# Performance work log

Hardware: AMD Instinct MI355X
Metric: run time of the kernel (lower is better)

## Reference

```python
import jax, jax.numpy as jnp
import numpy as np

B, S, T = 32, 64, 64          # batch, src_len, tgt_len
E = 1024                      # embedding_dim
H = 512                       # encoder hidden per direction
H2 = 2 * H                    # decoder hidden = enc_output_dim = 1024
VS, VT = 32000, 32000         # src / tgt vocab
L_ENC, L_DEC = 2, 2


def setup_inputs() -> dict:
    key = jax.random.key(0)
    ks = jax.random.split(key, 16)
    s = 0.05
    return {
        # tokens in [1, V) -> no pad tokens, all src_lens == S
        "x": jax.random.randint(ks[0], (B, S), 1, VS),
        "y": jax.random.randint(ks[1], (B, T), 1, VT),
        "src_emb": jax.random.normal(ks[2], (VS, E), jnp.float32) * s,
        "tgt_emb": jax.random.normal(ks[3], (VT, E), jnp.float32) * s,
        # encoder weights: [layer, dir(0=fwd,1=bwd), 4H, in] with in = E = 2H
        "enc_W_ih": jax.random.normal(ks[4], (L_ENC, 2, 4 * H, E), jnp.float32) * s,
        "enc_W_hh": jax.random.normal(ks[5], (L_ENC, 2, 4 * H, H), jnp.float32) * s,
        "enc_b_ih": jax.random.normal(ks[6], (L_ENC, 2, 4 * H), jnp.float32) * s,
        "enc_b_hh": jax.random.normal(ks[7], (L_ENC, 2, 4 * H), jnp.float32) * s,
        # decoder LSTMCells: cell0 input = E + H2 = 2048, cell1 input = H2
        "dec_W_ih0": jax.random.normal(ks[8], (4 * H2, E + H2), jnp.float32) * s,
        "dec_W_ih1": jax.random.normal(ks[9], (4 * H2, H2), jnp.float32) * s,
        "dec_W_hh": jax.random.normal(ks[10], (L_DEC, 4 * H2, H2), jnp.float32) * s,
        "dec_b_ih": jax.random.normal(ks[11], (L_DEC, 4 * H2), jnp.float32) * s,
        "dec_b_hh": jax.random.normal(ks[12], (L_DEC, 4 * H2), jnp.float32) * s,
        "W_out": jax.random.normal(ks[13], (VT, H2), jnp.float32) * s,
        "b_out": jax.random.normal(ks[14], (VT,), jnp.float32) * s,
    }


def _lstm_cell(x, h, c, W_ih, W_hh, b):
    # PyTorch gate order: i, f, g, o
    gates = x @ W_ih.T + h @ W_hh.T + b
    i, f, g, o = jnp.split(gates, 4, axis=-1)
    c2 = jax.nn.sigmoid(f) * c + jax.nn.sigmoid(i) * jnp.tanh(g)
    h2 = jax.nn.sigmoid(o) * jnp.tanh(c2)
    return h2, c2


def _run_dir(xseq, W_ih, W_hh, b):
    # xseq: [T, B, D] -> outputs [T, B, H], final (h, c)
    Bn, Hn = xseq.shape[1], W_hh.shape[1]
    init = (jnp.zeros((Bn, Hn), xseq.dtype), jnp.zeros((Bn, Hn), xseq.dtype))
    def step(carry, xt):
        h, c = carry
        h2, c2 = _lstm_cell(xt, h, c, W_ih, W_hh, b)
        return (h2, c2), h2
    (hT, cT), ys = jax.lax.scan(step, init, xseq)
    return ys, hT, cT


def _forward(x, y, src_emb, tgt_emb, enc_W_ih, enc_W_hh, enc_b_ih, enc_b_hh,
             dec_W_ih0, dec_W_ih1, dec_W_hh, dec_b_ih, dec_b_hh, W_out, b_out):
    # All src lengths are full -> per-row flip == full flip (pack is a no-op).
    x_rev = jnp.flip(x, axis=1)
    seq = src_emb[x_rev].transpose(1, 0, 2)  # [S, B, E]; dropout=0 (eval)

    h_fin, c_fin = [], []
    for l in range(L_ENC):
        b_f = enc_b_ih[l, 0] + enc_b_hh[l, 0]
        b_b = enc_b_ih[l, 1] + enc_b_hh[l, 1]
        ys_f, hT_f, cT_f = _run_dir(seq, enc_W_ih[l, 0], enc_W_hh[l, 0], b_f)
        ys_b, hT_b, cT_b = _run_dir(seq[::-1], enc_W_ih[l, 1], enc_W_hh[l, 1], b_b)
        seq = jnp.concatenate([ys_f, ys_b[::-1]], axis=-1)  # [S, B, 2H]
        h_fin.append(jnp.concatenate([hT_f, hT_b], axis=-1))  # [B, 2H]
        c_fin.append(jnp.concatenate([cT_f, cT_b], axis=-1))

    context = h_fin[-1]  # cat(hidden[-2], hidden[-1]) = last-layer fwd||bwd

    db0 = dec_b_ih[0] + dec_b_hh[0]
    db1 = dec_b_ih[1] + dec_b_hh[1]
    emb_seq = tgt_emb[y[:, :-1]].transpose(1, 0, 2)  # [T-1, B, E] teacher forcing

    def dec_step(carry, emb_t):
        h0, c0, h1, c1 = carry
        inp0 = jnp.concatenate([emb_t, context], axis=-1)
        h0, c0 = _lstm_cell(inp0, h0, c0, dec_W_ih0, dec_W_hh[0], db0)
        h1, c1 = _lstm_cell(h0, h1, c1, dec_W_ih1, dec_W_hh[1], db1)
        logit = h1 @ W_out.T + b_out
        return (h0, c0, h1, c1), logit

    init = (h_fin[0], c_fin[0], h_fin[1], c_fin[1])
    _, logits = jax.lax.scan(dec_step, init, emb_seq)  # [T-1, B, VT]
    return logits.transpose(1, 0, 2)  # [B, T-1, VT]


def reference(x, y, src_emb, tgt_emb, enc_W_ih, enc_W_hh, enc_b_ih, enc_b_hh,
              dec_W_ih0, dec_W_ih1, dec_W_hh, dec_b_ih, dec_b_hh, W_out, b_out):
    return _forward(x, y, src_emb, tgt_emb, enc_W_ih, enc_W_hh, enc_b_ih, enc_b_hh,
                    dec_W_ih0, dec_W_ih1, dec_W_hh, dec_b_ih, dec_b_hh, W_out, b_out)
```

## Files before the change

### kernel.cpp

```cpp
#include <hip/hip_runtime.h>

typedef __attribute__((ext_vector_type(8))) short short8;
typedef __attribute__((ext_vector_type(4))) float f32x4;

#define DEVINL __device__ __forceinline__

DEVINL unsigned short f2bf(float f) {
  unsigned int u = __builtin_bit_cast(unsigned int, f);
  unsigned int r = u + 0x7FFFu + ((u >> 16) & 1u);
  return (unsigned short)(r >> 16);
}
DEVINL float bf2f(unsigned short u) {
  unsigned int x = ((unsigned int)u) << 16;
  return __builtin_bit_cast(float, x);
}
DEVINL float sig_(float x) { return 1.f / (1.f + __expf(-x)); }
DEVINL float tanh_(float x) { return 2.f / (1.f + __expf(-2.f * x)) - 1.f; }

DEVINL void gld16(void* lds, const void* g) {
  __builtin_amdgcn_global_load_lds(
      (const __attribute__((address_space(1))) unsigned int*)g,
      (__attribute__((address_space(3))) unsigned int*)lds, 16, 0, 0);
}

DEVINL void coh_st(unsigned long long* p, unsigned long long v) {
  __hip_atomic_store(p, v, __ATOMIC_RELAXED, __HIP_MEMORY_SCOPE_AGENT);
}

DEVINL unsigned long long pack4w(unsigned int u, int lane, int s0, int s1) {
  unsigned int p1 = (unsigned int)__shfl_xor((int)u, s0);
  unsigned int lo2 = (lane & s0) ? ((p1 & 0xFFFFu) | (u << 16))
                                 : ((u & 0xFFFFu) | (p1 << 16));
  unsigned int p2 = (unsigned int)__shfl_xor((int)lo2, s1);
  unsigned int lo = (lane & s1) ? p2 : lo2;
  unsigned int hi = (lane & s1) ? lo2 : p2;
  return ((unsigned long long)hi << 32) | lo;
}

DEVINL void bar_arrive(int* arr, int idx, int gen) {
  if (threadIdx.x == 0)
    __hip_atomic_store(arr + idx, gen, __ATOMIC_RELAXED, __HIP_MEMORY_SCOPE_AGENT);
}
DEVINL void bar_wait(const int* arr, int nb, int gen) {
  if (threadIdx.x < 64) {
    for (;;) {
      int ok = 1;
      for (int i = (int)threadIdx.x; i < nb; i += 64)
        ok &= (__hip_atomic_load(arr + i, __ATOMIC_RELAXED, __HIP_MEMORY_SCOPE_AGENT) >= gen)
                  ? 1
                  : 0;
      if (__all(ok)) break;
      __builtin_amdgcn_s_sleep(2);
    }
  }
  __builtin_amdgcn_sched_barrier(0);
  asm volatile("" ::: "memory");
  __syncthreads();
}

__global__ __launch_bounds__(256) void gemm_bf16(
    const unsigned short* __restrict__ A, const unsigned short* __restrict__ Bt,
    void* __restrict__ C, const float* __restrict__ bias,
    int K, int N, int Mvalid, int mode) {
  __shared__ unsigned short lA[1024 * 8];
  __shared__ unsigned short lB[1024 * 8];
  const int tid = threadIdx.x;
  const int lane = tid & 63, wid = tid >> 6;
  const int wm = wid >> 1, wn = wid & 1;
  const int bm = blockIdx.x, bn = blockIdx.y;
  const size_t K_ = (size_t)K;

  const unsigned short* gAc[4];
  const unsigned short* gBc[4];
  unsigned short* lAc[4];
  unsigned short* lBc[4];
#pragma unroll
  for (int c = 0; c < 4; c++) {
    const int s = c * 256 + tid;
    const int r = s & 127, kb = s >> 7;
    gAc[c] = A + (size_t)(bm * 128 + r) * K_ + kb * 8;
    gBc[c] = Bt + (size_t)(bn * 128 + r) * K_ + kb * 8;
    lAc[c] = lA + (size_t)(c * 256 + wid * 64) * 8;
    lBc[c] = lB + (size_t)(c * 256 + wid * 64) * 8;
  }

  f32x4 acc[4][4] = {};
  const int kg = lane >> 4, lr = lane & 15;

  for (int kt = 0; kt < K; kt += 64) {
#pragma unroll
    for (int c = 0; c < 4; c++) {
      gld16(lAc[c], gAc[c] + kt);
      gld16(lBc[c], gBc[c] + kt);
    }
    __syncthreads();
#pragma unroll
    for (int ks = 0; ks < 2; ks++) {
      const int kgi = ks * 4 + kg;
      short8 af[4], bfr[4];
#pragma unroll
      for (int fm = 0; fm < 4; fm++)
        af[fm] = *(const short8*)&lA[(size_t)(kgi * 128 + wm * 64 + fm * 16 + lr) * 8];
#pragma unroll
      for (int fn = 0; fn < 4; fn++)
        bfr[fn] = *(const short8*)&lB[(size_t)(kgi * 128 + wn * 64 + fn * 16 + lr) * 8];
#pragma unroll
      for (int fm = 0; fm < 4; fm++)
#pragma unroll
        for (int fn = 0; fn < 4; fn++)
          acc[fm][fn] =
              __builtin_amdgcn_mfma_f32_16x16x32_bf16(af[fm], bfr[fn], acc[fm][fn], 0, 0, 0);
    }
    __syncthreads();
  }

#pragma unroll
  for (int fn = 0; fn < 4; fn++) {
    const int col = bn * 128 + wn * 64 + fn * 16 + lr;
    const float bv = bias ? bias[col] : 0.f;
#pragma unroll
    for (int fm = 0; fm < 4; fm++) {
      const int row0 = bm * 128 + wm * 64 + fm * 16 + kg * 4;
#pragma unroll
      for (int r = 0; r < 4; r++) {
        const int m = row0 + r;
        if (m < Mvalid) {
          const float v = acc[fm][fn][r] + bv;
          if (mode == 0) {
            ((float*)C)[(size_t)m * N + col] = v;
          } else if (mode == 1) {
            const int b = m & 31, t = m >> 5;
            ((float*)C)[(size_t)b * 2016000 + (size_t)t * 32000 + col] = v;
          } else {
            ((unsigned short*)C)[(size_t)m * N + col] = f2bf(v);
          }
        }
      }
    }
  }
}

__global__ __launch_bounds__(128, 1) void enc_chain(
    const unsigned short* __restrict__ Whh, const unsigned short* __restrict__ G,
    unsigned short* __restrict__ Henc, unsigned short* __restrict__ seq_out,
    float* __restrict__ c_out, int* bar) {
  extern __shared__ unsigned short lw[];
  const int tid = threadIdx.x, lane = tid & 63, w = tid >> 6;
  const int lr = lane & 15, kg = lane >> 4;
  const int dir = (int)blockIdx.x >> 4, j0 = ((int)blockIdx.x & 15) * 32;
  int* arr = bar + dir * 64;
  const int aidx = (int)blockIdx.x & 15;
  const unsigned short* Wd = Whh + (size_t)dir * 2048 * 512;
  for (int it = 0; it < 64; it++) {
    const int idx = (it * 128 + tid) * 16;
    const int r = idx >> 10, o = idx & 1023;
    const unsigned short* src = Wd + (size_t)((r >> 5) * 512 + j0 + (r & 31)) * 512 + (o >> 1);
    *(short8*)((char*)lw + r * 1024 + (o ^ ((r & 7) << 4))) = *(const short8*)src;
  }
  float cc[2][4] = {};
  float gpre[4][2][4];
  auto fetch_g = [&](int t) {
    const int s_idx = dir ? (63 - t) : t;
#pragma unroll
    for (int r = 0; r < 4; r++) {
      const unsigned short* Gr =
          G + (size_t)(s_idx * 32 + (w * 16 + kg * 4 + r)) * 4096 + dir * 2048;
#pragma unroll
      for (int jh = 0; jh < 2; jh++) {
        const int jj = j0 + jh * 16 + lr;
        gpre[r][jh][0] = bf2f(Gr[jj]);
        gpre[r][jh][1] = bf2f(Gr[512 + jj]);
        gpre[r][jh][2] = bf2f(Gr[1024 + jj]);
        gpre[r][jh][3] = bf2f(Gr[1536 + jj]);
      }
    }
  };
  fetch_g(0);
  __syncthreads();
  for (int t = 0; t < 64; t++) {
    const unsigned short* hA =
        Henc + ((size_t)(t * 2 + dir) * 32 + w * 16 + lr) * 512 + kg * 8;
    short8 areg[16];
#pragma unroll
    for (int kc = 0; kc < 16; kc++) areg[kc] = *(const short8*)(hA + kc * 32);
    f32x4 acc[8] = {};
#pragma unroll
    for (int kc = 0; kc < 16; kc++)
#pragma unroll
      for (int nt = 0; nt < 8; nt++) {
        const int rr = nt * 16 + lr;
        short8 bf = *(const short8*)((const char*)lw + rr * 1024 +
                                     ((kc * 64 + kg * 16) ^ ((rr & 7) << 4)));
        acc[nt] = __builtin_amdgcn_mfma_f32_16x16x32_bf16(areg[kc], bf, acc[nt], 0, 0, 0);
      }
    const int s_idx = dir ? (63 - t) : t;
    unsigned long long* HWU =
        (unsigned long long*)Henc + ((size_t)((t + 1) * 2 + dir) * 32) * 128;
#pragma unroll
    for (int r = 0; r < 4; r++) {
      const int b = w * 16 + kg * 4 + r;
#pragma unroll
      for (int jh = 0; jh < 2; jh++) {
        const float gi = gpre[r][jh][0] + acc[jh + 0][r];
        const float gf = gpre[r][jh][1] + acc[jh + 2][r];
        const float gg = gpre[r][jh][2] + acc[jh + 4][r];
        const float go = gpre[r][jh][3] + acc[jh + 6][r];
        const float cn = sig_(gf) * cc[jh][r] + sig_(gi) * tanh_(gg);
        const float hn = sig_(go) * tanh_(cn);
        cc[jh][r] = cn;
        unsigned long long pk = pack4w((unsigned int)f2bf(hn), lane, 1, 2);
        if ((lane & 3) == 0) {
          const int jjb = j0 + jh * 16 + lr;
          coh_st(HWU + b * 128 + (jjb >> 2), pk);
          if (seq_out)
            *(unsigned long long*)&seq_out[(size_t)(s_idx * 32 + b) * 1024 + dir * 512 +
                                           jjb] = pk;
        }
      }
    }
    if (t < 63) {
      __syncthreads();
      bar_arrive(arr, aidx, t + 1);
      fetch_g(t + 1);
      bar_wait(arr, 16, t + 1);
    }
  }
#pragma unroll
  for (int r = 0; r < 4; r++)
#pragma unroll
    for (int jh = 0; jh < 2; jh++)
      c_out[(dir * 32 + (w * 16 + kg * 4 + r)) * 512 + j0 + jh * 16 + lr] = cc[jh][r];
}

__global__ __launch_bounds__(128, 1) void dec_pipe(
    const unsigned short* __restrict__ Whh0, const unsigned short* __restrict__ Wc1,
    const unsigned short* __restrict__ G, const float* __restrict__ db1,
    const float* __restrict__ c0init, const float* __restrict__ c1init,
    unsigned short* __restrict__ H0ext, unsigned short* __restrict__ H1ext,
    int* bar) {
  extern __shared__ unsigned short lw[];
  const int tid = threadIdx.x, lane = tid & 63, w = tid >> 6;
  const int lr = lane & 15, kg = lane >> 4;
  const int bid = (int)blockIdx.x;

  if (bid < 64) {
    const int j0 = bid * 16, j = j0 + lr;
    for (int it = 0; it < 64; it++) {
      const int idx = (it * 128 + tid) * 16;
      const int r = idx >> 11, o = idx & 2047;
      const unsigned short* src =
          Whh0 + (size_t)((r >> 4) * 1024 + j0 + (r & 15)) * 1024 + (o >> 1);
      *(short8*)((char*)lw + r * 2048 + (o ^ ((r & 7) << 4))) = *(const short8*)src;
    }
    float cc[4];
#pragma unroll
    for (int r = 0; r < 4; r++) cc[r] = c0init[(w * 16 + kg * 4 + r) * 1024 + j];
    float gpre[4][4];
    auto fetch_g = [&](int k) {
#pragma unroll
      for (int r = 0; r < 4; r++) {
        const unsigned short* Gr = G + (size_t)(k * 32 + (w * 16 + kg * 4 + r)) * 4096 + j;
        gpre[r][0] = bf2f(Gr[0]);
        gpre[r][1] = bf2f(Gr[1024]);
        gpre[r][2] = bf2f(Gr[2048]);
        gpre[r][3] = bf2f(Gr[3072]);
      }
    };
    fetch_g(0);
    __syncthreads();
    for (int k = 0; k < 64; k++) {
      if (k < 63) {
        const unsigned short* hA = H0ext + ((size_t)k * 32 + w * 16 + lr) * 1024 + kg * 8;
        short8 areg[32];
#pragma unroll
        for (int kc = 0; kc < 32; kc++) areg[kc] = *(const short8*)(hA + kc * 32);
        f32x4 acc[4] = {};
#pragma unroll
        for (int kc = 0; kc < 32; kc++)
#pragma unroll
          for (int g = 0; g < 4; g++) {
            const int rr = g * 16 + lr;
            short8 bf = *(const short8*)((const char*)lw + rr * 2048 +
                                         ((kc * 64 + kg * 16) ^ ((rr & 7) << 4)));
            acc[g] = __builtin_amdgcn_mfma_f32_16x16x32_bf16(areg[kc], bf, acc[g], 0, 0, 0);
          }
        unsigned long long* HWU = (unsigned long long*)H0ext + ((size_t)(k + 1) * 32) * 256;
#pragma unroll
        for (int r = 0; r < 4; r++) {
          const int b = w * 16 + kg * 4 + r;
          const float gi = gpre[r][0] + acc[0][r];
          const float gf = gpre[r][1] + acc[1][r];
          const float gg = gpre[r][2] + acc[2][r];
          const float go = gpre[r][3] + acc[3][r];
          const float cn = sig_(gf) * cc[r] + sig_(gi) * tanh_(gg);
          const float hn = sig_(go) * tanh_(cn);
          cc[r] = cn;
          unsigned long long pk = pack4w((unsigned int)f2bf(hn), lane, 1, 2);
          if ((lane & 3) == 0)
            coh_st(HWU + b * 256 + ((j0 + lr) >> 2), pk);
        }
      }
      if (k < 63) {
        __syncthreads();
        bar_arrive(bar, bid, k + 1);
        if (k < 62) fetch_g(k + 1);
        bar_wait(bar, 192, k + 1);
      }
    }
  } else {
    const int j0 = (bid - 64) * 8;
    for (int it = 0; it < 64; it++) {
      const int idx = (it * 128 + tid) * 16;
      const int r = idx >> 12, o = idx & 4095;
      const unsigned short* src =
          Wc1 + (size_t)((r & 3) * 1024 + j0 + (r >> 2)) * 2048 + (o >> 1);
      *(short8*)((char*)lw + r * 4096 + (o ^ ((r & 7) << 4))) = *(const short8*)src;
    }
    float cc[2][4];
    float bb1[2][4];
#pragma unroll
    for (int n = 0; n < 2; n++) {
      const int j = j0 + n * 4 + (lr >> 2);
#pragma unroll
      for (int g = 0; g < 4; g++) bb1[n][g] = db1[g * 1024 + j];
#pragma unroll
      for (int r = 0; r < 4; r++)
        cc[n][r] = c1init[(w * 16 + kg * 4 + r) * 1024 + j];
    }
    __syncthreads();
    for (int k = 0; k < 64; k++) {
      if (k >= 1) {
        f32x4 acc[2] = {};
        {
          const unsigned short* hA = H0ext + ((size_t)k * 32 + w * 16 + lr) * 1024 + kg * 8;
          short8 areg[32];
#pragma unroll
          for (int kc = 0; kc < 32; kc++) areg[kc] = *(const short8*)(hA + kc * 32);
#pragma unroll
          for (int kc = 0; kc < 32; kc++)
#pragma unroll
            for (int n = 0; n < 2; n++) {
              const int rr = n * 16 + lr;
              short8 bf = *(const short8*)((const char*)lw + rr * 4096 +
                                           ((kc * 64 + kg * 16) ^ ((rr & 7) << 4)));
              acc[n] = __builtin_amdgcn_mfma_f32_16x16x32_bf16(areg[kc], bf, acc[n], 0, 0, 0);
            }
        }
        {
          const unsigned short* hA =
              H1ext + ((size_t)(k - 1) * 32 + w * 16 + lr) * 1024 + kg * 8;
          short8 areg[32];
#pragma unroll
          for (int kc = 0; kc < 32; kc++) areg[kc] = *(const short8*)(hA + kc * 32);
#pragma unroll
          for (int kc = 32; kc < 64; kc++)
#pragma unroll
            for (int n = 0; n < 2; n++) {
              const int rr = n * 16 + lr;
              short8 bf = *(const short8*)((const char*)lw + rr * 4096 +
                                           ((kc * 64 + kg * 16) ^ ((rr & 7) << 4)));
              acc[n] = __builtin_amdgcn_mfma_f32_16x16x32_bf16(areg[kc - 32], bf, acc[n],
                                                               0, 0, 0);
            }
        }
        unsigned long long* HWU = (unsigned long long*)H1ext + ((size_t)k * 32) * 256;
#pragma unroll
        for (int n = 0; n < 2; n++) {
#pragma unroll
          for (int r = 0; r < 4; r++) {
            const int b = w * 16 + kg * 4 + r;
            const float v = acc[n][r];
            const float e1a = __shfl_xor(v, 1);
            const float e0 = (lane & 1) ? e1a : v;
            const float e1 = (lane & 1) ? v : e1a;
            const float f0 = __shfl_xor(e0, 2), f1 = __shfl_xor(e1, 2);
            const float gi = ((lane & 2) ? f0 : e0) + bb1[n][0];
            const float gf = ((lane & 2) ? f1 : e1) + bb1[n][1];
            const float gg = ((lane & 2) ? e0 : f0) + bb1[n][2];
            const float go = ((lane & 2) ? e1 : f1) + bb1[n][3];
            const float cn = sig_(gf) * cc[n][r] + sig_(gi) * tanh_(gg);
            const float hn = sig_(go) * tanh_(cn);
            cc[n][r] = cn;
            unsigned long long pk = pack4w((unsigned int)f2bf(hn), lane, 4, 8);
            if ((lane & 15) == 0)
              coh_st(HWU + b * 256 + ((j0 + n * 4) >> 2), pk);
          }
        }
      }
      if (k < 63) {
        __syncthreads();
        bar_arrive(bar, bid, k + 1);
        bar_wait(bar, 192, k + 1);
      }
    }
  }
}

__global__ void cvt_bf16(const float* __restrict__ in, unsigned short* __restrict__ out,
                         long n4) {
  long i = (long)blockIdx.x * blockDim.x + threadIdx.x;
  const long stride = (long)gridDim.x * blockDim.x;
  for (; i < n4; i += stride) {
    f32x4 v = *(const f32x4*)&in[i * 4];
    ushort4 o = {f2bf(v.x), f2bf(v.y), f2bf(v.z), f2bf(v.w)};
    *(ushort4*)&out[i * 4] = o;
  }
}

__global__ void pack_wc1(const float* __restrict__ Wih1, const float* __restrict__ Whh1,
                         unsigned short* __restrict__ Wc) {
  const int n = blockIdx.x;
  const int c = threadIdx.x * 8;
  const float* src = (c < 1024) ? (Wih1 + (size_t)n * 1024 + c)
                                : (Whh1 + (size_t)n * 1024 + (c - 1024));
  f32x4 v0 = *(const f32x4*)src;
  f32x4 v1 = *(const f32x4*)(src + 4);
  ushort4 o0 = {f2bf(v0.x), f2bf(v0.y), f2bf(v0.z), f2bf(v0.w)};
  ushort4 o1 = {f2bf(v1.x), f2bf(v1.y), f2bf(v1.z), f2bf(v1.w)};
  *(ushort4*)&Wc[(size_t)n * 2048 + c] = o0;
  *(ushort4*)&Wc[(size_t)n * 2048 + c + 4] = o1;
}

__global__ void bias_comb(const float* __restrict__ a, const float* __restrict__ b,
                          float* __restrict__ out, int n) {
  int i = blockIdx.x * blockDim.x + threadIdx.x;
  if (i < n) out[i] = a[i] + b[i];
}

__global__ void embed_src(const int* __restrict__ x, const float* __restrict__ emb,
                          unsigned short* __restrict__ A0) {
  const int row = blockIdx.x;
  const int s = row >> 5, b = row & 31;
  const int tok = x[b * 64 + (63 - s)];
  const int col = threadIdx.x * 4;
  f32x4 v = *(const f32x4*)(emb + (size_t)tok * 1024 + col);
  ushort4 o = {f2bf(v.x), f2bf(v.y), f2bf(v.z), f2bf(v.w)};
  *(ushort4*)&A0[(size_t)row * 1024 + col] = o;
}

__global__ void embed_tgt(const int* __restrict__ y, const float* __restrict__ emb,
                          unsigned short* __restrict__ inp0) {
  const int row = blockIdx.x;
  const int col = threadIdx.x * 4;
  ushort4 o = {0, 0, 0, 0};
  if (row < 2016) {
    const int t = row >> 5, b = row & 31;
    const int tok = y[b * 64 + t];
    f32x4 v = *(const f32x4*)(emb + (size_t)tok * 1024 + col);
    o = ushort4{f2bf(v.x), f2bf(v.y), f2bf(v.z), f2bf(v.w)};
  } else {
    *(ushort4*)&inp0[(size_t)row * 2048 + 1024 + col] = o;
  }
  *(ushort4*)&inp0[(size_t)row * 2048 + col] = o;
}

__global__ void fill_ctx2(const unsigned short* __restrict__ Hl1,
                          unsigned short* __restrict__ inp0) {
  const int row = blockIdx.x;
  const int b = row & 31;
  const int col = threadIdx.x * 4;
  const int dir = col >> 9, jj = col & 511;
  ushort4 v = *(const ushort4*)(Hl1 + ((size_t)dir * 32 + b) * 512 + jj);
  *(ushort4*)&inp0[(size_t)row * 2048 + 1024 + col] = v;
}

__global__ void dec_init2(const unsigned short* __restrict__ Hl0,
                          const unsigned short* __restrict__ Hl1,
                          const float* __restrict__ Cl0, const float* __restrict__ Cl1,
                          unsigned short* __restrict__ H0e, unsigned short* __restrict__ H1e,
                          float* __restrict__ c0, float* __restrict__ c1) {
  const int i = blockIdx.x * 256 + threadIdx.x;
  const int b = i >> 10, col = i & 1023;
  const int dir = col >> 9, jj = col & 511;
  const int se = (dir * 32 + b) * 512 + jj;
  const int de = b * 1024 + col;
  H0e[de] = Hl0[se];
  H1e[de] = Hl1[se];
  c0[de] = Cl0[se];
  c1[de] = Cl1[se];
}

extern "C" void kernel_launch(void* const* d_in, const int* in_sizes, int n_in,
                              void* d_out, int out_size, void* d_ws, size_t ws_size,
                              hipStream_t stream) {
  const int* x = (const int*)d_in[0];
  const int* y = (const int*)d_in[1];
  const float* src_emb = (const float*)d_in[2];
  const float* tgt_emb = (const float*)d_in[3];
  const float* enc_W_ih = (const float*)d_in[4];
  const float* enc_W_hh = (const float*)d_in[5];
  const float* enc_b_ih = (const float*)d_in[6];
  const float* enc_b_hh = (const float*)d_in[7];
  const float* dec_W_ih0 = (const float*)d_in[8];
  const float* dec_W_ih1 = (const float*)d_in[9];
  const float* dec_W_hh = (const float*)d_in[10];
  const float* dec_b_ih = (const float*)d_in[11];
  const float* dec_b_hh = (const float*)d_in[12];
  const float* W_out = (const float*)d_in[13];
  const float* b_out = (const float*)d_in[14];
  float* out = (float*)d_out;

  char* ws = (char*)d_ws;
  size_t off = 0;
  auto alloc = [&](size_t bytes) -> void* {
    void* p = ws + off;
    off += (bytes + 255) & ~(size_t)255;
    return p;
  };
  unsigned short* A0 = (unsigned short*)alloc(2048ull * 1024 * 2);
  unsigned short* seq1 = (unsigned short*)alloc(2048ull * 1024 * 2);
  unsigned short* Wih_bf = (unsigned short*)alloc(2ull * 4096 * 1024 * 2);
  unsigned short* Wih0_bf = (unsigned short*)alloc(4096ull * 2048 * 2);
  unsigned short* Wout_bf = (unsigned short*)alloc(32000ull * 1024 * 2);
  unsigned short* G = (unsigned short*)alloc(2048ull * 4096 * 2);
  unsigned short* inp0 = (unsigned short*)alloc(2048ull * 2048 * 2);
  unsigned short* Whh_enc_bf = (unsigned short*)alloc(2ull * 2 * 2048 * 512 * 2);
  unsigned short* Whh0_bf = (unsigned short*)alloc(4096ull * 1024 * 2);
  unsigned short* Wc1_bf = (unsigned short*)alloc(4096ull * 2048 * 2);
  unsigned short* H0ext = (unsigned short*)alloc(2080ull * 1024 * 2);
  unsigned short* H1ext = (unsigned short*)alloc(2080ull * 1024 * 2);
  unsigned short* Henc0 = (unsigned short*)alloc(65ull * 2 * 32 * 512 * 2);
  unsigned short* Henc1 = (unsigned short*)alloc(65ull * 2 * 32 * 512 * 2);
  float* encbias = (float*)alloc(2ull * 4096 * 4);
  float* decdb = (float*)alloc(2ull * 4096 * 4);
  float* c_l0 = (float*)alloc(2ull * 32 * 512 * 4);
  float* c_l1 = (float*)alloc(2ull * 32 * 512 * 4);
  float* c0buf = (float*)alloc(32ull * 1024 * 4);
  float* c1buf = (float*)alloc(32ull * 1024 * 4);
  int* bar = (int*)alloc(512 * 4);
  if (off > ws_size) return;

  (void)hipFuncSetAttribute((const void*)enc_chain,
                            hipFuncAttributeMaxDynamicSharedMemorySize, 131072);
  (void)hipFuncSetAttribute((const void*)dec_pipe,
                            hipFuncAttributeMaxDynamicSharedMemorySize, 131072);

  cvt_bf16<<<1024, 256, 0, stream>>>(enc_W_ih, Wih_bf, (2ll * 4096 * 1024) / 4);
  cvt_bf16<<<1024, 256, 0, stream>>>(dec_W_ih0, Wih0_bf, (4096ll * 2048) / 4);
  cvt_bf16<<<2048, 256, 0, stream>>>(W_out, Wout_bf, (32000ll * 1024) / 4);
  cvt_bf16<<<1024, 256, 0, stream>>>(enc_W_hh, Whh_enc_bf, (2ll * 2 * 2048 * 512) / 4);
  cvt_bf16<<<1024, 256, 0, stream>>>(dec_W_hh, Whh0_bf, (4096ll * 1024) / 4);
  pack_wc1<<<4096, 256, 0, stream>>>(dec_W_ih1, dec_W_hh + 4096ll * 1024, Wc1_bf);
  bias_comb<<<32, 256, 0, stream>>>(enc_b_ih, enc_b_hh, encbias, 8192);
  bias_comb<<<32, 256, 0, stream>>>(dec_b_ih, dec_b_hh, decdb, 8192);
  embed_src<<<2048, 256, 0, stream>>>(x, src_emb, A0);
  embed_tgt<<<2048, 256, 0, stream>>>(y, tgt_emb, inp0);
  hipMemsetAsync(Henc0, 0, 2ull * 32 * 512 * 2, stream);
  hipMemsetAsync(Henc1, 0, 2ull * 32 * 512 * 2, stream);
  hipMemsetAsync(bar, 0, 512 * 4, stream);

  gemm_bf16<<<dim3(16, 32), 256, 0, stream>>>(A0, Wih_bf, G, encbias, 1024, 4096, 2048, 2);
  enc_chain<<<32, 128, 131072, stream>>>(Whh_enc_bf, G, Henc0, seq1, c_l0, bar + 0);
  gemm_bf16<<<dim3(16, 32), 256, 0, stream>>>(seq1, Wih_bf + 4096ull * 1024, G,
                                              encbias + 4096, 1024, 4096, 2048, 2);
  enc_chain<<<32, 128, 131072, stream>>>(Whh_enc_bf + 2ull * 2048 * 512, G, Henc1, nullptr,
                                         c_l1, bar + 128);

  dec_init2<<<128, 256, 0, stream>>>(Henc0 + 64ull * 2 * 32 * 512,
                                     Henc1 + 64ull * 2 * 32 * 512, c_l0, c_l1,
                                     H0ext, H1ext, c0buf, c1buf);
  fill_ctx2<<<2016, 256, 0, stream>>>(Henc1 + 64ull * 2 * 32 * 512, inp0);
  gemm_bf16<<<dim3(16, 32), 256, 0, stream>>>(inp0, Wih0_bf, G, decdb, 2048, 4096, 2048, 2);

  dec_pipe<<<192, 128, 131072, stream>>>(Whh0_bf, Wc1_bf, G, decdb + 4096, c0buf, c1buf,
                                         H0ext, H1ext, bar + 256);

  gemm_bf16<<<dim3(16, 250), 256, 0, stream>>>(H1ext + 32ull * 1024, Wout_bf, out, b_out,
                                               1024, 32000, 2016, 1);
}
```

Before: 2.243 ms.

## Fuse decoder recurrence with output projection via work queue and producer-consumer flags

Merges the decoder pipeline kernel and the vocabulary projection GEMM into one persistent kernel. The single global barrier across all 192 blocks becomes per-layer progress flags: layer-1 blocks wait only on layer-0 progress and their own layer. All 256 blocks then pull output tiles from an atomic queue, each waiting only until the needed timesteps of H1 exist, so the logits GEMM overlaps the serial recurrence. Blocks now run 256 threads while only 128 do the recurrence math, and the whole kernel depends on every block being co-resident.

```diff
diff --git a/kernel.cpp b/kernel.cpp
--- a/kernel.cpp
+++ b/kernel.cpp
@@ -41,12 +41,32 @@
   if (threadIdx.x == 0)
     __hip_atomic_store(arr + idx, gen, __ATOMIC_RELAXED, __HIP_MEMORY_SCOPE_AGENT);
 }
-DEVINL void bar_wait(const int* arr, int nb, int gen) {
+DEVINL void wait1(const int* arr, int nb, int gen) {
   if (threadIdx.x < 64) {
     for (;;) {
       int ok = 1;
       for (int i = (int)threadIdx.x; i < nb; i += 64)
         ok &= (__hip_atomic_load(arr + i, __ATOMIC_RELAXED, __HIP_MEMORY_SCOPE_AGENT) >= gen)
+                  ? 1
+                  : 0;
+      if (__all(ok)) break;
+      __builtin_amdgcn_s_sleep(2);
+    }
+  }
+  __builtin_amdgcn_sched_barrier(0);
+  asm volatile("" ::: "memory");
+  __syncthreads();
+}
+DEVINL void wait2(const int* a0, int n0, int g0, const int* a1, int n1, int g1) {
+  if (threadIdx.x < 64) {
+    for (;;) {
+      int ok = 1;
+      for (int i = (int)threadIdx.x; i < n0; i += 64)
+        ok &= (__hip_atomic_load(a0 + i, __ATOMIC_RELAXED, __HIP_MEMORY_SCOPE_AGENT) >= g0)
+                  ? 1
+                  : 0;
+      for (int i = (int)threadIdx.x; i < n1; i += 64)
+        ok &= (__hip_atomic_load(a1 + i, __ATOMIC_RELAXED, __HIP_MEMORY_SCOPE_AGENT) >= g1)
                   ? 1
                   : 0;
       if (__all(ok)) break;
@@ -222,7 +242,7 @@
       __syncthreads();
       bar_arrive(arr, aidx, t + 1);
       fetch_g(t + 1);
-      bar_wait(arr, 16, t + 1);
+      wait1(arr, 16, t + 1);
     }
   }
 #pragma unroll
@@ -232,29 +252,32 @@
       c_out[(dir * 32 + (w * 16 + kg * 4 + r)) * 512 + j0 + jh * 16 + lr] = cc[jh][r];
 }
 
-__global__ __launch_bounds__(128, 1) void dec_pipe(
+__global__ __launch_bounds__(256, 1) void dec_logits(
     const unsigned short* __restrict__ Whh0, const unsigned short* __restrict__ Wc1,
     const unsigned short* __restrict__ G, const float* __restrict__ db1,
     const float* __restrict__ c0init, const float* __restrict__ c1init,
     unsigned short* __restrict__ H0ext, unsigned short* __restrict__ H1ext,
-    int* bar) {
+    const unsigned short* __restrict__ Wout, float* __restrict__ out,
+    const float* __restrict__ b_out, int* bar) {
   extern __shared__ unsigned short lw[];
+  __shared__ int wq;
   const int tid = threadIdx.x, lane = tid & 63, w = tid >> 6;
   const int lr = lane & 15, kg = lane >> 4;
   const int bid = (int)blockIdx.x;
+  int* arr0 = bar;
+  int* arr1 = bar + 128;
+  int* qidx = bar + 512;
 
   if (bid < 64) {
     const int j0 = bid * 16, j = j0 + lr;
-    for (int it = 0; it < 64; it++) {
-      const int idx = (it * 128 + tid) * 16;
+    for (int it = 0; it < 32; it++) {
+      const int idx = (it * 256 + tid) * 16;
       const int r = idx >> 11, o = idx & 2047;
       const unsigned short* src =
           Whh0 + (size_t)((r >> 4) * 1024 + j0 + (r & 15)) * 1024 + (o >> 1);
       *(short8*)((char*)lw + r * 2048 + (o ^ ((r & 7) << 4))) = *(const short8*)src;
     }
-    float cc[4];
-#pragma unroll
-    for (int r = 0; r < 4; r++) cc[r] = c0init[(w * 16 + kg * 4 + r) * 1024 + j];
+    float cc[4] = {};
     float gpre[4][4];
     auto fetch_g = [&](int k) {
 #pragma unroll
@@ -266,10 +289,15 @@
         gpre[r][3] = bf2f(Gr[3072]);
       }
     };
-    fetch_g(0);
+    if (tid < 128) {
+#pragma unroll
+      for (int r = 0; r < 4; r++) cc[r] = c0init[(w * 16 + kg * 4 + r) * 1024 + j];
+      fetch_g(0);
+    }
     __syncthreads();
-    for (int k = 0; k < 64; k++) {
-      if (k < 63) {
+    for (int k = 0; k < 63; k++) {
+      if (k > 0) wait1(arr0, 64, k);
+      if (tid < 128) {
         const unsigned short* hA = H0ext + ((size_t)k * 32 + w * 16 + lr) * 1024 + kg * 8;
         short8 areg[32];
 #pragma unroll
@@ -300,39 +328,40 @@
             coh_st(HWU + b * 256 + ((j0 + lr) >> 2), pk);
         }
       }
-      if (k < 63) {
-        __syncthreads();
-        bar_arrive(bar, bid, k + 1);
-        if (k < 62) fetch_g(k + 1);
-        bar_wait(bar, 192, k + 1);
-      }
-    }
-  } else {
+      __syncthreads();
+      bar_arrive(arr0, bid, k + 1);
+      if (tid < 128 && k < 62) fetch_g(k + 1);
+    }
+  } else if (bid < 192) {
     const int j0 = (bid - 64) * 8;
-    for (int it = 0; it < 64; it++) {
-      const int idx = (it * 128 + tid) * 16;
+    for (int it = 0; it < 32; it++) {
+      const int idx = (it * 256 + tid) * 16;
       const int r = idx >> 12, o = idx & 4095;
       const unsigned short* src =
           Wc1 + (size_t)((r & 3) * 1024 + j0 + (r >> 2)) * 2048 + (o >> 1);
       *(short8*)((char*)lw + r * 4096 + (o ^ ((r & 7) << 4))) = *(const short8*)src;
     }
-    float cc[2][4];
-    float bb1[2][4];
-#pragma unroll
-    for (int n = 0; n < 2; n++) {
-      const int j = j0 + n * 4 + (lr >> 2);
-#pragma unroll
-      for (int g = 0; g < 4; g++) bb1[n][g] = db1[g * 1024 + j];
-#pragma unroll
-      for (int r = 0; r < 4; r++)
-        cc[n][r] = c1init[(w * 16 + kg * 4 + r) * 1024 + j];
+    float cc[2][4] = {};
+    float bb1[2][4] = {};
+    if (tid < 128) {
+#pragma unroll
+      for (int n = 0; n < 2; n++) {
+        const int j = j0 + n * 4 + (lr >> 2);
+#pragma unroll
+        for (int g = 0; g < 4; g++) bb1[n][g] = db1[g * 1024 + j];
+#pragma unroll
+        for (int r = 0; r < 4; r++)
+          cc[n][r] = c1init[(w * 16 + kg * 4 + r) * 1024 + j];
+      }
     }
     __syncthreads();
-    for (int k = 0; k < 64; k++) {
-      if (k >= 1) {
+    for (int t = 0; t < 63; t++) {
+      wait2(arr0, 64, t + 1, arr1, 128, t);
+      if (tid < 128) {
         f32x4 acc[2] = {};
         {
-          const unsigned short* hA = H0ext + ((size_t)k * 32 + w * 16 + lr) * 1024 + kg * 8;
+          const unsigned short* hA =
+              H0ext + ((size_t)(t + 1) * 32 + w * 16 + lr) * 1024 + kg * 8;
           short8 areg[32];
 #pragma unroll
           for (int kc = 0; kc < 32; kc++) areg[kc] = *(const short8*)(hA + kc * 32);
@@ -347,8 +376,7 @@
             }
         }
         {
-          const unsigned short* hA =
-              H1ext + ((size_t)(k - 1) * 32 + w * 16 + lr) * 1024 + kg * 8;
+          const unsigned short* hA = H1ext + ((size_t)t * 32 + w * 16 + lr) * 1024 + kg * 8;
           short8 areg[32];
 #pragma unroll
           for (int kc = 0; kc < 32; kc++) areg[kc] = *(const short8*)(hA + kc * 32);
@@ -363,7 +391,7 @@
                                                                0, 0, 0);
             }
         }
-        unsigned long long* HWU = (unsigned long long*)H1ext + ((size_t)k * 32) * 256;
+        unsigned long long* HWU = (unsigned long long*)H1ext + ((size_t)(t + 1) * 32) * 256;
 #pragma unroll
         for (int n = 0; n < 2; n++) {
 #pragma unroll
@@ -387,10 +415,73 @@
           }
         }
       }
-      if (k < 63) {
+      __syncthreads();
+      bar_arrive(arr1, bid - 64, t + 1);
+    }
+  }
+
+  {
+    const unsigned short* Abase = H1ext + 32ull * 1024;
+    unsigned short* lA = lw;
+    unsigned short* lB = lw + 8192;
+    const int wid = tid >> 6, wm = wid >> 1, wn = wid & 1;
+    for (;;) {
+      __syncthreads();
+      if (tid == 0) wq = atomicAdd(qidx, 1);
+      __syncthreads();
+      const int wk = wq;
+      if (wk >= 4000) break;
+      const int mt = wk / 250, nb = wk % 250;
+      const int need = (4 * mt + 4 < 63) ? (4 * mt + 4) : 63;
+      wait1(arr1, 128, need);
+
+      f32x4 acc[4][4] = {};
+      for (int kt = 0; kt < 1024; kt += 64) {
+#pragma unroll
+        for (int c = 0; c < 4; c++) {
+          const int s = c * 256 + tid;
+          const int r = s & 127, kb = s >> 7;
+          gld16(lA + (size_t)(c * 256 + wid * 64) * 8,
+                Abase + (size_t)(mt * 128 + r) * 1024 + kb * 8 + kt);
+          gld16(lB + (size_t)(c * 256 + wid * 64) * 8,
+                Wout + (size_t)(nb * 128 + r) * 1024 + kb * 8 + kt);
+        }
         __syncthreads();
-        bar_arrive(bar, bid, k + 1);
-        bar_wait(bar, 192, k + 1);
+#pragma unroll
+        for (int ks = 0; ks < 2; ks++) {
+          const int kgi = ks * 4 + kg;
+          short8 af[4], bfr[4];
+#pragma unroll
+          for (int fm = 0; fm < 4; fm++)
+            af[fm] = *(const short8*)&lA[(size_t)(kgi * 128 + wm * 64 + fm * 16 + lr) * 8];
+#pragma unroll
+          for (int fn = 0; fn < 4; fn++)
+            bfr[fn] = *(const short8*)&lB[(size_t)(kgi * 128 + wn * 64 + fn * 16 + lr) * 8];
+#pragma unroll
+          for (int fm = 0; fm < 4; fm++)
+#pragma unroll
+            for (int fn = 0; fn < 4; fn++)
+              acc[fm][fn] = __builtin_amdgcn_mfma_f32_16x16x32_bf16(af[fm], bfr[fn],
+                                                                    acc[fm][fn], 0, 0, 0);
+        }
+        __syncthreads();
+      }
+#pragma unroll
+      for (int fn = 0; fn < 4; fn++) {
+        const int col = nb * 128 + wn * 64 + fn * 16 + lr;
+        const float bv = b_out[col];
+#pragma unroll
+        for (int fm = 0; fm < 4; fm++) {
+          const int row0 = mt * 128 + wm * 64 + fm * 16 + kg * 4;
+#pragma unroll
+          for (int r = 0; r < 4; r++) {
+            const int m = row0 + r;
+            if (m < 2016) {
+              const int b = m & 31, t = m >> 5;
+              out[(size_t)b * 2016000 + (size_t)t * 32000 + col] = acc[fm][fn][r] + bv;
+            }
+          }
+        }
       }
     }
   }
@@ -527,12 +618,12 @@
   float* c_l1 = (float*)alloc(2ull * 32 * 512 * 4);
   float* c0buf = (float*)alloc(32ull * 1024 * 4);
   float* c1buf = (float*)alloc(32ull * 1024 * 4);
-  int* bar = (int*)alloc(512 * 4);
+  int* bar = (int*)alloc(1024 * 4);
   if (off > ws_size) return;
 
   (void)hipFuncSetAttribute((const void*)enc_chain,
                             hipFuncAttributeMaxDynamicSharedMemorySize, 131072);
-  (void)hipFuncSetAttribute((const void*)dec_pipe,
+  (void)hipFuncSetAttribute((const void*)dec_logits,
                             hipFuncAttributeMaxDynamicSharedMemorySize, 131072);
 
   cvt_bf16<<<1024, 256, 0, stream>>>(enc_W_ih, Wih_bf, (2ll * 4096 * 1024) / 4);
@@ -547,14 +638,14 @@
   embed_tgt<<<2048, 256, 0, stream>>>(y, tgt_emb, inp0);
   hipMemsetAsync(Henc0, 0, 2ull * 32 * 512 * 2, stream);
   hipMemsetAsync(Henc1, 0, 2ull * 32 * 512 * 2, stream);
-  hipMemsetAsync(bar, 0, 512 * 4, stream);
+  hipMemsetAsync(bar, 0, 1024 * 4, stream);
 
   gemm_bf16<<<dim3(16, 32), 256, 0, stream>>>(A0, Wih_bf, G, encbias, 1024, 4096, 2048, 2);
   enc_chain<<<32, 128, 131072, stream>>>(Whh_enc_bf, G, Henc0, seq1, c_l0, bar + 0);
   gemm_bf16<<<dim3(16, 32), 256, 0, stream>>>(seq1, Wih_bf + 4096ull * 1024, G,
                                               encbias + 4096, 1024, 4096, 2048, 2);
   enc_chain<<<32, 128, 131072, stream>>>(Whh_enc_bf + 2ull * 2048 * 512, G, Henc1, nullptr,
-                                         c_l1, bar + 128);
+                                         c_l1, bar + 640);
 
   dec_init2<<<128, 256, 0, stream>>>(Henc0 + 64ull * 2 * 32 * 512,
                                      Henc1 + 64ull * 2 * 32 * 512, c_l0, c_l1,
@@ -562,9 +653,6 @@
   fill_ctx2<<<2016, 256, 0, stream>>>(Henc1 + 64ull * 2 * 32 * 512, inp0);
   gemm_bf16<<<dim3(16, 32), 256, 0, stream>>>(inp0, Wih0_bf, G, decdb, 2048, 4096, 2048, 2);
 
-  dec_pipe<<<192, 128, 131072, stream>>>(Whh0_bf, Wc1_bf, G, decdb + 4096, c0buf, c1buf,
-                                         H0ext, H1ext, bar + 256);
-
-  gemm_bf16<<<dim3(16, 250), 256, 0, stream>>>(H1ext + 32ull * 1024, Wout_bf, out, b_out,
-                                               1024, 32000, 2016, 1);
-}
+  dec_logits<<<256, 256, 131072, stream>>>(Whh0_bf, Wc1_bf, G, decdb + 4096, c0buf, c1buf,
+                                           H0ext, H1ext, Wout_bf, out, b_out, bar + 256);
+}
```

After: 2.721 ms. 21.3% more time.

## Decouple decoder layer barriers and split K across two wave-pairs per block

Applied to the files above, without the earlier changes.

The decoder pipeline drops its single all-block barrier. It now uses two flag arrays, so layer-0 blocks wait only on layer-0 peers and layer-1 blocks wait on the layer-0 step they consume plus their own layer. The two layers can then run skewed instead of in lockstep. Each block grows to 256 threads, and the K reduction is split between two thread halves that are combined through extra LDS, which shortens each step's serial MFMA chain. Barrier flags are padded to separate cache lines to cut contention, at the cost of more LDS per block and an extra intra-block sync and reduction every step.

```diff
diff --git a/kernel.cpp b/kernel.cpp
--- a/kernel.cpp
+++ b/kernel.cpp
@@ -39,14 +39,37 @@
 
 DEVINL void bar_arrive(int* arr, int idx, int gen) {
   if (threadIdx.x == 0)
-    __hip_atomic_store(arr + idx, gen, __ATOMIC_RELAXED, __HIP_MEMORY_SCOPE_AGENT);
-}
-DEVINL void bar_wait(const int* arr, int nb, int gen) {
+    __hip_atomic_store(arr + idx * 16, gen, __ATOMIC_RELAXED, __HIP_MEMORY_SCOPE_AGENT);
+}
+DEVINL void wait1(const int* arr, int nb, int gen) {
   if (threadIdx.x < 64) {
     for (;;) {
       int ok = 1;
       for (int i = (int)threadIdx.x; i < nb; i += 64)
-        ok &= (__hip_atomic_load(arr + i, __ATOMIC_RELAXED, __HIP_MEMORY_SCOPE_AGENT) >= gen)
+        ok &= (__hip_atomic_load(arr + i * 16, __ATOMIC_RELAXED,
+                                 __HIP_MEMORY_SCOPE_AGENT) >= gen)
+                  ? 1
+                  : 0;
+      if (__all(ok)) break;
+      __builtin_amdgcn_s_sleep(2);
+    }
+  }
+  __builtin_amdgcn_sched_barrier(0);
+  asm volatile("" ::: "memory");
+  __syncthreads();
+}
+DEVINL void wait2(const int* a0, int n0, int g0, const int* a1, int n1, int g1) {
+  if (threadIdx.x < 64) {
+    for (;;) {
+      int ok = 1;
+      for (int i = (int)threadIdx.x; i < n0; i += 64)
+        ok &= (__hip_atomic_load(a0 + i * 16, __ATOMIC_RELAXED,
+                                 __HIP_MEMORY_SCOPE_AGENT) >= g0)
+                  ? 1
+                  : 0;
+      for (int i = (int)threadIdx.x; i < n1; i += 64)
+        ok &= (__hip_atomic_load(a1 + i * 16, __ATOMIC_RELAXED,
+                                 __HIP_MEMORY_SCOPE_AGENT) >= g1)
                   ? 1
                   : 0;
       if (__all(ok)) break;
@@ -148,7 +171,7 @@
   const int tid = threadIdx.x, lane = tid & 63, w = tid >> 6;
   const int lr = lane & 15, kg = lane >> 4;
   const int dir = (int)blockIdx.x >> 4, j0 = ((int)blockIdx.x & 15) * 32;
-  int* arr = bar + dir * 64;
+  int* arr = bar + dir * 256;
   const int aidx = (int)blockIdx.x & 15;
   const unsigned short* Wd = Whh + (size_t)dir * 2048 * 512;
   for (int it = 0; it < 64; it++) {
@@ -222,7 +245,7 @@
       __syncthreads();
       bar_arrive(arr, aidx, t + 1);
       fetch_g(t + 1);
-      bar_wait(arr, 16, t + 1);
+      wait1(arr, 16, t + 1);
     }
   }
 #pragma unroll
@@ -232,66 +255,83 @@
       c_out[(dir * 32 + (w * 16 + kg * 4 + r)) * 512 + j0 + jh * 16 + lr] = cc[jh][r];
 }
 
-__global__ __launch_bounds__(128, 1) void dec_pipe(
+__global__ __launch_bounds__(256, 1) void dec_pipe(
     const unsigned short* __restrict__ Whh0, const unsigned short* __restrict__ Wc1,
     const unsigned short* __restrict__ G, const float* __restrict__ db1,
     const float* __restrict__ c0init, const float* __restrict__ c1init,
     unsigned short* __restrict__ H0ext, unsigned short* __restrict__ H1ext,
-    int* bar) {
+    int* arr0, int* arr1) {
   extern __shared__ unsigned short lw[];
-  const int tid = threadIdx.x, lane = tid & 63, w = tid >> 6;
+  f32x4* red4 = (f32x4*)((char*)lw + 131072);
+  const int tid = threadIdx.x, lane = tid & 63;
   const int lr = lane & 15, kg = lane >> 4;
+  const int wv = (tid >> 6) & 1, half = tid >> 7;
   const int bid = (int)blockIdx.x;
 
   if (bid < 64) {
     const int j0 = bid * 16, j = j0 + lr;
-    for (int it = 0; it < 64; it++) {
-      const int idx = (it * 128 + tid) * 16;
+    for (int it = 0; it < 32; it++) {
+      const int idx = (it * 256 + tid) * 16;
       const int r = idx >> 11, o = idx & 2047;
       const unsigned short* src =
           Whh0 + (size_t)((r >> 4) * 1024 + j0 + (r & 15)) * 1024 + (o >> 1);
       *(short8*)((char*)lw + r * 2048 + (o ^ ((r & 7) << 4))) = *(const short8*)src;
     }
-    float cc[4];
-#pragma unroll
-    for (int r = 0; r < 4; r++) cc[r] = c0init[(w * 16 + kg * 4 + r) * 1024 + j];
+    float cc[4] = {};
     float gpre[4][4];
     auto fetch_g = [&](int k) {
 #pragma unroll
       for (int r = 0; r < 4; r++) {
-        const unsigned short* Gr = G + (size_t)(k * 32 + (w * 16 + kg * 4 + r)) * 4096 + j;
+        const unsigned short* Gr = G + (size_t)(k * 32 + (wv * 16 + kg * 4 + r)) * 4096 + j;
         gpre[r][0] = bf2f(Gr[0]);
         gpre[r][1] = bf2f(Gr[1024]);
         gpre[r][2] = bf2f(Gr[2048]);
         gpre[r][3] = bf2f(Gr[3072]);
       }
     };
-    fetch_g(0);
+    if (tid < 128) {
+#pragma unroll
+      for (int r = 0; r < 4; r++) cc[r] = c0init[(wv * 16 + kg * 4 + r) * 1024 + j];
+      fetch_g(0);
+    }
     __syncthreads();
-    for (int k = 0; k < 64; k++) {
-      if (k < 63) {
-        const unsigned short* hA = H0ext + ((size_t)k * 32 + w * 16 + lr) * 1024 + kg * 8;
-        short8 areg[32];
-#pragma unroll
-        for (int kc = 0; kc < 32; kc++) areg[kc] = *(const short8*)(hA + kc * 32);
-        f32x4 acc[4] = {};
-#pragma unroll
-        for (int kc = 0; kc < 32; kc++)
-#pragma unroll
-          for (int g = 0; g < 4; g++) {
-            const int rr = g * 16 + lr;
-            short8 bf = *(const short8*)((const char*)lw + rr * 2048 +
-                                         ((kc * 64 + kg * 16) ^ ((rr & 7) << 4)));
-            acc[g] = __builtin_amdgcn_mfma_f32_16x16x32_bf16(areg[kc], bf, acc[g], 0, 0, 0);
-          }
+    for (int k = 0; k < 63; k++) {
+      if (k > 0) wait1(arr0, 64, k);
+      const unsigned short* hA =
+          H0ext + ((size_t)k * 32 + wv * 16 + lr) * 1024 + half * 512 + kg * 8;
+      short8 areg[16];
+#pragma unroll
+      for (int kcl = 0; kcl < 16; kcl++) areg[kcl] = *(const short8*)(hA + kcl * 32);
+      f32x4 acc[4] = {};
+#pragma unroll
+      for (int kcl = 0; kcl < 16; kcl++) {
+        const int kc = half * 16 + kcl;
+#pragma unroll
+        for (int g = 0; g < 4; g++) {
+          const int rr = g * 16 + lr;
+          short8 bf = *(const short8*)((const char*)lw + rr * 2048 +
+                                       ((kc * 64 + kg * 16) ^ ((rr & 7) << 4)));
+          acc[g] = __builtin_amdgcn_mfma_f32_16x16x32_bf16(areg[kcl], bf, acc[g], 0, 0, 0);
+        }
+      }
+      if (half == 1) {
+#pragma unroll
+        for (int g = 0; g < 4; g++) red4[g * 128 + wv * 64 + lane] = acc[g];
+      }
+      __syncthreads();
+      if (tid < 128) {
         unsigned long long* HWU = (unsigned long long*)H0ext + ((size_t)(k + 1) * 32) * 256;
 #pragma unroll
         for (int r = 0; r < 4; r++) {
-          const int b = w * 16 + kg * 4 + r;
-          const float gi = gpre[r][0] + acc[0][r];
-          const float gf = gpre[r][1] + acc[1][r];
-          const float gg = gpre[r][2] + acc[2][r];
-          const float go = gpre[r][3] + acc[3][r];
+          const int b = wv * 16 + kg * 4 + r;
+          f32x4 a0 = red4[0 * 128 + wv * 64 + lane];
+          f32x4 a1 = red4[1 * 128 + wv * 64 + lane];
+          f32x4 a2 = red4[2 * 128 + wv * 64 + lane];
+          f32x4 a3 = red4[3 * 128 + wv * 64 + lane];
+          const float gi = gpre[r][0] + acc[0][r] + a0[r];
+          const float gf = gpre[r][1] + acc[1][r] + a1[r];
+          const float gg = gpre[r][2] + acc[2][r] + a2[r];
+          const float go = gpre[r][3] + acc[3][r] + a3[r];
           const float cn = sig_(gf) * cc[r] + sig_(gi) * tanh_(gg);
           const float hn = sig_(go) * tanh_(cn);
           cc[r] = cn;
@@ -300,76 +340,67 @@
             coh_st(HWU + b * 256 + ((j0 + lr) >> 2), pk);
         }
       }
-      if (k < 63) {
-        __syncthreads();
-        bar_arrive(bar, bid, k + 1);
-        if (k < 62) fetch_g(k + 1);
-        bar_wait(bar, 192, k + 1);
-      }
+      __syncthreads();
+      bar_arrive(arr0, bid, k + 1);
+      if (tid < 128 && k < 62) fetch_g(k + 1);
     }
   } else {
     const int j0 = (bid - 64) * 8;
-    for (int it = 0; it < 64; it++) {
-      const int idx = (it * 128 + tid) * 16;
+    for (int it = 0; it < 32; it++) {
+      const int idx = (it * 256 + tid) * 16;
       const int r = idx >> 12, o = idx & 4095;
       const unsigned short* src =
           Wc1 + (size_t)((r & 3) * 1024 + j0 + (r >> 2)) * 2048 + (o >> 1);
       *(short8*)((char*)lw + r * 4096 + (o ^ ((r & 7) << 4))) = *(const short8*)src;
     }
-    float cc[2][4];
-    float bb1[2][4];
-#pragma unroll
-    for (int n = 0; n < 2; n++) {
-      const int j = j0 + n * 4 + (lr >> 2);
-#pragma unroll
-      for (int g = 0; g < 4; g++) bb1[n][g] = db1[g * 1024 + j];
-#pragma unroll
-      for (int r = 0; r < 4; r++)
-        cc[n][r] = c1init[(w * 16 + kg * 4 + r) * 1024 + j];
+    float cc[2][4] = {};
+    float bb1[2][4] = {};
+    if (tid < 128) {
+#pragma unroll
+      for (int n = 0; n < 2; n++) {
+        const int j = j0 + n * 4 + (lr >> 2);
+#pragma unroll
+        for (int g = 0; g < 4; g++) bb1[n][g] = db1[g * 1024 + j];
+#pragma unroll
+        for (int r = 0; r < 4; r++)
+          cc[n][r] = c1init[(wv * 16 + kg * 4 + r) * 1024 + j];
+      }
     }
     __syncthreads();
-    for (int k = 0; k < 64; k++) {
-      if (k >= 1) {
-        f32x4 acc[2] = {};
-        {
-          const unsigned short* hA = H0ext + ((size_t)k * 32 + w * 16 + lr) * 1024 + kg * 8;
-          short8 areg[32];
-#pragma unroll
-          for (int kc = 0; kc < 32; kc++) areg[kc] = *(const short8*)(hA + kc * 32);
-#pragma unroll
-          for (int kc = 0; kc < 32; kc++)
-#pragma unroll
-            for (int n = 0; n < 2; n++) {
-              const int rr = n * 16 + lr;
-              short8 bf = *(const short8*)((const char*)lw + rr * 4096 +
-                                           ((kc * 64 + kg * 16) ^ ((rr & 7) << 4)));
-              acc[n] = __builtin_amdgcn_mfma_f32_16x16x32_bf16(areg[kc], bf, acc[n], 0, 0, 0);
-            }
+    for (int t = 0; t < 63; t++) {
+      wait2(arr0, 64, t + 1, arr1, 128, t);
+      const unsigned short* hA =
+          half ? (H1ext + ((size_t)t * 32 + wv * 16 + lr) * 1024 + kg * 8)
+               : (H0ext + ((size_t)(t + 1) * 32 + wv * 16 + lr) * 1024 + kg * 8);
+      short8 areg[32];
+#pragma unroll
+      for (int kcl = 0; kcl < 32; kcl++) areg[kcl] = *(const short8*)(hA + kcl * 32);
+      f32x4 acc[2] = {};
+#pragma unroll
+      for (int kcl = 0; kcl < 32; kcl++) {
+        const int kc = half * 32 + kcl;
+#pragma unroll
+        for (int n = 0; n < 2; n++) {
+          const int rr = n * 16 + lr;
+          short8 bf = *(const short8*)((const char*)lw + rr * 4096 +
+                                       ((kc * 64 + kg * 16) ^ ((rr & 7) << 4)));
+          acc[n] = __builtin_amdgcn_mfma_f32_16x16x32_bf16(areg[kcl], bf, acc[n], 0, 0, 0);
         }
-        {
-          const unsigned short* hA =
-              H1ext + ((size_t)(k - 1) * 32 + w * 16 + lr) * 1024 + kg * 8;
-          short8 areg[32];
-#pragma unroll
-          for (int kc = 0; kc < 32; kc++) areg[kc] = *(const short8*)(hA + kc * 32);
-#pragma unroll
-          for (int kc = 32; kc < 64; kc++)
-#pragma unroll
-            for (int n = 0; n < 2; n++) {
-              const int rr = n * 16 + lr;
-              short8 bf = *(const short8*)((const char*)lw + rr * 4096 +
-                                           ((kc * 64 + kg * 16) ^ ((rr & 7) << 4)));
-              acc[n] = __builtin_amdgcn_mfma_f32_16x16x32_bf16(areg[kc - 32], bf, acc[n],
-                                                               0, 0, 0);
-            }
-        }
-        unsigned long long* HWU = (unsigned long long*)H1ext + ((size_t)k * 32) * 256;
+      }
+      if (half == 1) {
+#pragma unroll
+        for (int n = 0; n < 2; n++) red4[n * 128 + wv * 64 + lane] = acc[n];
+      }
+      __syncthreads();
+      if (tid < 128) {
+        unsigned long long* HWU = (unsigned long long*)H1ext + ((size_t)(t + 1) * 32) * 256;
 #pragma unroll
         for (int n = 0; n < 2; n++) {
+          f32x4 ar = red4[n * 128 + wv * 64 + lane];
 #pragma unroll
           for (int r = 0; r < 4; r++) {
-            const int b = w * 16 + kg * 4 + r;
-            const float v = acc[n][r];
+            const int b = wv * 16 + kg * 4 + r;
+            const float v = acc[n][r] + ar[r];
             const float e1a = __shfl_xor(v, 1);
             const float e0 = (lane & 1) ? e1a : v;
             const float e1 = (lane & 1) ? v : e1a;
@@ -387,11 +418,8 @@
           }
         }
       }
-      if (k < 63) {
-        __syncthreads();
-        bar_arrive(bar, bid, k + 1);
-        bar_wait(bar, 192, k + 1);
-      }
+      __syncthreads();
+      bar_arrive(arr1, bid - 64, t + 1);
     }
   }
 }
@@ -527,13 +555,13 @@
   float* c_l1 = (float*)alloc(2ull * 32 * 512 * 4);
   float* c0buf = (float*)alloc(32ull * 1024 * 4);
   float* c1buf = (float*)alloc(32ull * 1024 * 4);
-  int* bar = (int*)alloc(512 * 4);
+  int* bar = (int*)alloc(4096 * 4);
   if (off > ws_size) return;
 
   (void)hipFuncSetAttribute((const void*)enc_chain,
                             hipFuncAttributeMaxDynamicSharedMemorySize, 131072);
   (void)hipFuncSetAttribute((const void*)dec_pipe,
-                            hipFuncAttributeMaxDynamicSharedMemorySize, 131072);
+                            hipFuncAttributeMaxDynamicSharedMemorySize, 139264);
 
   cvt_bf16<<<1024, 256, 0, stream>>>(enc_W_ih, Wih_bf, (2ll * 4096 * 1024) / 4);
   cvt_bf16<<<1024, 256, 0, stream>>>(dec_W_ih0, Wih0_bf, (4096ll * 2048) / 4);
@@ -547,14 +575,14 @@
   embed_tgt<<<2048, 256, 0, stream>>>(y, tgt_emb, inp0);
   hipMemsetAsync(Henc0, 0, 2ull * 32 * 512 * 2, stream);
   hipMemsetAsync(Henc1, 0, 2ull * 32 * 512 * 2, stream);
-  hipMemsetAsync(bar, 0, 512 * 4, stream);
+  hipMemsetAsync(bar, 0, 4096 * 4, stream);
 
   gemm_bf16<<<dim3(16, 32), 256, 0, stream>>>(A0, Wih_bf, G, encbias, 1024, 4096, 2048, 2);
   enc_chain<<<32, 128, 131072, stream>>>(Whh_enc_bf, G, Henc0, seq1, c_l0, bar + 0);
   gemm_bf16<<<dim3(16, 32), 256, 0, stream>>>(seq1, Wih_bf + 4096ull * 1024, G,
                                               encbias + 4096, 1024, 4096, 2048, 2);
   enc_chain<<<32, 128, 131072, stream>>>(Whh_enc_bf + 2ull * 2048 * 512, G, Henc1, nullptr,
-                                         c_l1, bar + 128);
+                                         c_l1, bar + 512);
 
   dec_init2<<<128, 256, 0, stream>>>(Henc0 + 64ull * 2 * 32 * 512,
                                      Henc1 + 64ull * 2 * 32 * 512, c_l0, c_l1,
@@ -562,8 +590,8 @@
   fill_ctx2<<<2016, 256, 0, stream>>>(Henc1 + 64ull * 2 * 32 * 512, inp0);
   gemm_bf16<<<dim3(16, 32), 256, 0, stream>>>(inp0, Wih0_bf, G, decdb, 2048, 4096, 2048, 2);
 
-  dec_pipe<<<192, 128, 131072, stream>>>(Whh0_bf, Wc1_bf, G, decdb + 4096, c0buf, c1buf,
-                                         H0ext, H1ext, bar + 256);
+  dec_pipe<<<192, 256, 139264, stream>>>(Whh0_bf, Wc1_bf, G, decdb + 4096, c0buf, c1buf,
+                                         H0ext, H1ext, bar + 1024, bar + 2048);
 
   gemm_bf16<<<dim3(16, 250), 256, 0, stream>>>(H1ext + 32ull * 1024, Wout_bf, out, b_out,
                                                1024, 32000, 2016, 1);
```

Result: faster. 2.163 ms (-3.6%).
